# Optimization experiments

Hardware: AMD Instinct MI355X
Metric: run time of the kernel (lower is better)

Reference implementation:

```python
import jax, jax.numpy as jnp
import numpy as np

B, S, E, H = 2, 2048, 1024, 16
D = E // H  # head_dim = 64


def setup_inputs() -> dict:
    key = jax.random.key(0)
    ks = jax.random.split(key, 9)
    sc = 1.0 / np.sqrt(E)
    return {
        "x": jax.random.normal(ks[0], (B, S, E), dtype=jnp.float32),
        "Wq": jax.random.normal(ks[1], (E, E), dtype=jnp.float32) * sc,
        "bq": jnp.zeros((E,), dtype=jnp.float32),
        "Wk": jax.random.normal(ks[2], (E, E), dtype=jnp.float32) * sc,
        "bk": jnp.zeros((E,), dtype=jnp.float32),
        "Wv": jax.random.normal(ks[3], (E, E), dtype=jnp.float32) * sc,
        "bv": jnp.zeros((E,), dtype=jnp.float32),
        "Wo": jax.random.normal(ks[4], (E, E), dtype=jnp.float32) * sc,
        "bo": jnp.zeros((E,), dtype=jnp.float32),
    }


def reference(x, Wq, bq, Wk, bk, Wv, bv, Wo, bo):
    b, s, e = x.shape
    # projections: [B,S,E] -> [B,H,S,D]
    def heads(w, bias):
        return (x @ w + bias).reshape(b, s, H, D).transpose(0, 2, 1, 3)
    q, k, v = heads(Wq, bq), heads(Wk, bk), heads(Wv, bv)
    # scores [B,H,S,S]
    scores = jnp.einsum("bhqd,bhkd->bhqk", q, k) / jnp.sqrt(jnp.float32(D))
    causal = jnp.tril(jnp.ones((s, s), dtype=bool))
    scores = jnp.where(causal[None, None], scores, -jnp.inf)
    weights = jax.nn.softmax(scores, axis=-1)
    out = jnp.einsum("bhqk,bhkd->bhqd", weights, v)
    out = out.transpose(0, 2, 1, 3).reshape(b, s, e)
    return out @ Wo + bo
```

## Files before the change

### kernel.cpp

```cpp
#include <hip/hip_runtime.h>
#include <hip/hip_bf16.h>

#define B_SZ 2
#define S_LEN 2048
#define E_DIM 1024
#define NH 16
#define DH 64
#define M_ROWS (B_SZ * S_LEN)
#define QB 128
#define KVB 64

typedef __attribute__((ext_vector_type(8))) short short8;
typedef __attribute__((ext_vector_type(4))) float floatx4;
typedef __attribute__((ext_vector_type(4))) int intx4;

static __device__ __forceinline__ unsigned short f2bf(float f) {
    __hip_bfloat16 h = __float2bfloat16(f);
    return *reinterpret_cast<unsigned short*>(&h);
}
static __device__ __forceinline__ float bf2f(unsigned short u) {
    unsigned int v = ((unsigned int)u) << 16;
    return __builtin_bit_cast(float, v);
}
static __device__ __forceinline__ unsigned int pack2bf(float lo, float hi) {
    return (unsigned int)f2bf(lo) | ((unsigned int)f2bf(hi) << 16);
}

static __device__ __forceinline__ void gl2lds16(const void* g, void* l) {
    __builtin_amdgcn_global_load_lds((const __attribute__((address_space(1))) void*)g,
                                     (__attribute__((address_space(3))) void*)l, 16, 0, 0);
}

#define WAIT_VM0() asm volatile("s_waitcnt vmcnt(0)" ::: "memory")
#define WAIT_LGKM0() asm volatile("s_waitcnt lgkmcnt(0)" ::: "memory")

__global__ __launch_bounds__(256) void prep(const float* __restrict__ x,
                                            unsigned short* __restrict__ Xb,
                                            const float* __restrict__ W0,
                                            const float* __restrict__ W1,
                                            const float* __restrict__ W2,
                                            const float* __restrict__ W3,
                                            unsigned short* __restrict__ T0,
                                            unsigned short* __restrict__ T1,
                                            unsigned short* __restrict__ T2,
                                            unsigned short* __restrict__ T3) {
    __shared__ float tile[32][33];
    int bid = blockIdx.x;
    int t = threadIdx.x;
    if (bid < 4096) {
        int i = (bid * 256 + t) * 4;
        float4 v = *reinterpret_cast<const float4*>(x + i);
        ushort4 o;
        o.x = f2bf(v.x); o.y = f2bf(v.y); o.z = f2bf(v.z); o.w = f2bf(v.w);
        *reinterpret_cast<ushort4*>(Xb + i) = o;
        return;
    }
    int u = bid - 4096;
    int z = u >> 10, rest = u & 1023;
    int bx = (rest & 31) * 32, by = (rest >> 5) * 32;
    const float* W = (z == 0) ? W0 : (z == 1) ? W1 : (z == 2) ? W2 : W3;
    unsigned short* Wt = (z == 0) ? T0 : (z == 1) ? T1 : (z == 2) ? T2 : T3;
    int tx = t & 31, ty = t >> 5;
#pragma unroll
    for (int i = 0; i < 32; i += 8)
        tile[ty + i][tx] = W[(size_t)(by + ty + i) * E_DIM + bx + tx];
    __syncthreads();
#pragma unroll
    for (int i = 0; i < 32; i += 8)
        Wt[(size_t)(bx + ty + i) * E_DIM + by + tx] = f2bf(tile[tx][ty + i]);
}

#define QSCALE 0.18033688011112042f

__global__ __launch_bounds__(512, 1) void gemm_qkv8(const unsigned short* __restrict__ Wcat,
                                                    const unsigned short* __restrict__ Xb,
                                                    const float* __restrict__ bq,
                                                    const float* __restrict__ bk,
                                                    const float* __restrict__ bv,
                                                    unsigned short* __restrict__ Qg,
                                                    unsigned short* __restrict__ Kg,
                                                    unsigned short* __restrict__ Vtg) {
    __shared__ __align__(16) char lds[2][57344];

    int t = threadIdx.x;
    int b = blockIdx.x;
    int xcd = b & 7, ii = b >> 3;
    int it = (xcd & 3) * 4 + (ii >> 3);
    int jt = (xcd >> 2) * 8 + (ii & 7);
    int iBase = it * 192, jBase = jt << 8;

    int w = t >> 6, lane = t & 63;
    int lr = lane & 15, lh = lane >> 4;
    int wm = w >> 2, wn = w & 3;

    int srow = t >> 3;
    int scbx = ((t & 7) << 4) ^ ((srow & 7) << 4);

    const char* Ab = (const char*)Wcat;
    const char* Bb = (const char*)Xb;

    floatx4 acc[6][4];
#pragma unroll
    for (int i = 0; i < 6; i++)
#pragma unroll
        for (int j = 0; j < 4; j++) acc[i][j] = (floatx4){0.f, 0.f, 0.f, 0.f};

    auto stageA = [&](int buf, int kt) {
        int k0b = kt << 7;
#pragma unroll
        for (int c = 0; c < 3; c++)
            gl2lds16(Ab + (size_t)(iBase + c * 64 + srow) * 2048 + k0b + scbx,
                     &lds[buf][c * 8192 + t * 16]);
    };
    auto stageB = [&](int buf, int kt) {
        int k0b = kt << 7;
#pragma unroll
        for (int c = 0; c < 4; c++)
            gl2lds16(Bb + (size_t)(jBase + c * 64 + srow) * 2048 + k0b + scbx,
                     &lds[buf][24576 + c * 8192 + t * 16]);
    };

    short8 af[3][2], bf[4][2];
    auto rdA = [&](int buf, int qm) {
#pragma unroll
        for (int ml = 0; ml < 3; ml++)
#pragma unroll
            for (int ks = 0; ks < 2; ks++) {
                int row = wm * 96 + (qm * 3 + ml) * 16 + lr;
                af[ml][ks] = *reinterpret_cast<const short8*>(
                    &lds[buf][(row * 128 + ks * 64 + lh * 16) ^ ((row & 7) << 4)]);
            }
    };
    auto rdB = [&](int buf, int qn) {
#pragma unroll
        for (int nl = 0; nl < 2; nl++)
#pragma unroll
            for (int ks = 0; ks < 2; ks++) {
                int row = wn * 64 + (qn * 2 + nl) * 16 + lr;
                bf[qn * 2 + nl][ks] = *reinterpret_cast<const short8*>(
                    &lds[buf][24576 + ((row * 128 + ks * 64 + lh * 16) ^ ((row & 7) << 4))]);
            }
    };
    auto mfma12 = [&](int qm, int qn) {
        __builtin_amdgcn_s_setprio(1);
#pragma unroll
        for (int ml = 0; ml < 3; ml++)
#pragma unroll
            for (int nl = 0; nl < 2; nl++)
#pragma unroll
                for (int ks = 0; ks < 2; ks++)
                    acc[qm * 3 + ml][qn * 2 + nl] = __builtin_amdgcn_mfma_f32_16x16x32_bf16(
                        af[ml][ks], bf[qn * 2 + nl][ks], acc[qm * 3 + ml][qn * 2 + nl], 0, 0, 0);
        __builtin_amdgcn_s_setprio(0);
    };

    const int NT = 16;
    stageA(0, 0);
    stageB(0, 0);
    WAIT_VM0();
    __builtin_amdgcn_s_barrier();

    for (int kt = 0; kt < NT; ++kt) {
        int cur = kt & 1, nxt = cur ^ 1;
        bool pf = (kt + 1 < NT);
        rdA(cur, 0);
        rdB(cur, 0);
        if (pf) stageA(nxt, kt + 1);
        __builtin_amdgcn_s_barrier();
        WAIT_LGKM0();
        __builtin_amdgcn_sched_barrier(0);
        mfma12(0, 0);
        __builtin_amdgcn_s_barrier();
        rdB(cur, 1);
        if (pf) stageB(nxt, kt + 1);
        __builtin_amdgcn_s_barrier();
        WAIT_LGKM0();
        __builtin_amdgcn_sched_barrier(0);
        mfma12(0, 1);
        __builtin_amdgcn_s_barrier();
        rdA(cur, 1);
        __builtin_amdgcn_s_barrier();
        WAIT_LGKM0();
        __builtin_amdgcn_sched_barrier(0);
        mfma12(1, 0);
        __builtin_amdgcn_s_barrier();
        if (pf) WAIT_VM0();
        __builtin_amdgcn_s_barrier();
        mfma12(1, 1);
        __builtin_amdgcn_s_barrier();
    }

    __syncthreads();
    unsigned short* vt = reinterpret_cast<unsigned short*>(&lds[0][0] + w * 2560);

#pragma unroll
    for (int mi = 0; mi < 6; mi++) {
        int i0 = iBase + wm * 96 + mi * 16;
        int wsel = i0 >> 10;
        int im = i0 & 1023;
        const float* bias = (wsel == 0) ? bq : (wsel == 1) ? bk : bv;
        float4 bs = *reinterpret_cast<const float4*>(&bias[im + lh * 4]);
        if (wsel < 2) {
            unsigned short* O = wsel ? Kg : Qg;
            float scale = wsel ? 1.0f : QSCALE;
            int h = im >> 6, d0 = (im & 63) + lh * 4;
#pragma unroll
            for (int nf = 0; nf < 4; nf++) {
                int j = jBase + wn * 64 + nf * 16 + lr;
                int b_ = j >> 11, s = j & (S_LEN - 1);
                ushort4 pk;
                pk.x = f2bf((acc[mi][nf][0] + bs.x) * scale);
                pk.y = f2bf((acc[mi][nf][1] + bs.y) * scale);
                pk.z = f2bf((acc[mi][nf][2] + bs.z) * scale);
                pk.w = f2bf((acc[mi][nf][3] + bs.w) * scale);
                *reinterpret_cast<ushort4*>(
                    &O[((size_t)(b_ * NH + h) * S_LEN + s) * DH + d0]) = pk;
            }
        } else {
#pragma unroll
            for (int nf = 0; nf < 4; nf++)
#pragma unroll
                for (int r = 0; r < 4; r++) {
                    float bb = (r == 0) ? bs.x : (r == 1) ? bs.y : (r == 2) ? bs.z : bs.w;
                    vt[(lh * 4 + r) * 80 + nf * 16 + lr] = f2bf(acc[mi][nf][r] + bb);
                }
            WAIT_LGKM0();
            __builtin_amdgcn_sched_barrier(0);
            int h = im >> 6, d0 = im & 63;
#pragma unroll
            for (int p = 0; p < 2; p++) {
                int idx = p * 64 + lane;
                int dl = idx >> 3, sg = idx & 7;
                short8 vv = *reinterpret_cast<const short8*>(&vt[dl * 80 + sg * 8]);
                int j = jBase + wn * 64 + sg * 8;
                int b_ = j >> 11, s = j & (S_LEN - 1);
                *reinterpret_cast<short8*>(
                    &Vtg[((size_t)(b_ * NH + h) * DH + d0 + dl) * S_LEN + s]) = vv;
            }
            WAIT_LGKM0();
            __builtin_amdgcn_sched_barrier(0);
        }
    }
}

__global__ __launch_bounds__(512, 2) void gemm_o8(const unsigned short* __restrict__ Wot,
                                                  const unsigned short* __restrict__ Og,
                                                  const float* __restrict__ bo,
                                                  float* __restrict__ out) {
    __shared__ __align__(16) char lds[2][2][16384];

    int t = threadIdx.x;
    int b = blockIdx.x;
    int xcd = b & 7, ii = b >> 3;
    int it = ii & 7;
    int jt = (xcd << 2) | (ii >> 3);
    int iBase = it << 7, jBase = jt << 7;

    int w = t >> 6, lane = t & 63;
    int lr = lane & 15, lh = lane >> 4;
    int wm = w >> 2, wn = w & 3;

    int srow = t >> 3;
    int scbx = ((t & 7) << 4) ^ ((srow & 7) << 4);

    const char* Ab = (const char*)Wot;
    const char* Bb = (const char*)Og;

    floatx4 acc[4][2];
#pragma unroll
    for (int i = 0; i < 4; i++)
#pragma unroll
        for (int j = 0; j < 2; j++) acc[i][j] = (floatx4){0.f, 0.f, 0.f, 0.f};

    auto stageA = [&](int buf, int kt) {
        int k0b = kt << 7;
#pragma unroll
        for (int c = 0; c < 2; c++)
            gl2lds16(Ab + (size_t)(iBase + c * 64 + srow) * 2048 + k0b + scbx,
                     &lds[buf][0][c * 8192 + t * 16]);
    };
    auto stageB = [&](int buf, int kt) {
        int k0b = kt << 7;
#pragma unroll
        for (int c = 0; c < 2; c++)
            gl2lds16(Bb + (size_t)(jBase + c * 64 + srow) * 2048 + k0b + scbx,
                     &lds[buf][1][c * 8192 + t * 16]);
    };

    short8 af[4][2], bf[2][2];
    auto rdA = [&](int buf, int qm) {
#pragma unroll
        for (int m2 = 0; m2 < 2; m2++)
#pragma unroll
            for (int ks = 0; ks < 2; ks++) {
                int mi = qm * 2 + m2;
                int row = wm * 64 + mi * 16 + lr;
                af[mi][ks] = *reinterpret_cast<const short8*>(
                    &lds[buf][0][(row * 128 + ks * 64 + lh * 16) ^ ((row & 7) << 4)]);
            }
    };
    auto rdB = [&](int buf) {
#pragma unroll
        for (int nf = 0; nf < 2; nf++)
#pragma unroll
            for (int ks = 0; ks < 2; ks++) {
                int row = wn * 32 + nf * 16 + lr;
                bf[nf][ks] = *reinterpret_cast<const short8*>(
                    &lds[buf][1][(row * 128 + ks * 64 + lh * 16) ^ ((row & 7) << 4)]);
            }
    };
    auto mfma8 = [&](int qm) {
        __builtin_amdgcn_s_setprio(1);
#pragma unroll
        for (int m2 = 0; m2 < 2; m2++)
#pragma unroll
            for (int nf = 0; nf < 2; nf++)
#pragma unroll
                for (int ks = 0; ks < 2; ks++) {
                    int mi = qm * 2 + m2;
                    acc[mi][nf] = __builtin_amdgcn_mfma_f32_16x16x32_bf16(
                        af[mi][ks], bf[nf][ks], acc[mi][nf], 0, 0, 0);
                }
        __builtin_amdgcn_s_setprio(0);
    };

    const int NT = 16;
    stageA(0, 0);
    stageB(0, 0);
    WAIT_VM0();
    __builtin_amdgcn_s_barrier();

    for (int kt = 0; kt < NT; ++kt) {
        int cur = kt & 1, nxt = cur ^ 1;
        bool pf = (kt + 1 < NT);
        rdA(cur, 0);
        rdB(cur);
        if (pf) stageA(nxt, kt + 1);
        __builtin_amdgcn_s_barrier();
        WAIT_LGKM0();
        __builtin_amdgcn_sched_barrier(0);
        mfma8(0);
        __builtin_amdgcn_s_barrier();
        rdA(cur, 1);
        if (pf) stageB(nxt, kt + 1);
        __builtin_amdgcn_s_barrier();
        WAIT_LGKM0();
        __builtin_amdgcn_sched_barrier(0);
        mfma8(1);
        if (pf) WAIT_VM0();
        __builtin_amdgcn_s_barrier();
    }

#pragma unroll
    for (int mi = 0; mi < 4; mi++) {
        int i = iBase + wm * 64 + mi * 16 + lh * 4;
        float4 bs = *reinterpret_cast<const float4*>(&bo[i]);
#pragma unroll
        for (int nf = 0; nf < 2; nf++) {
            int j = jBase + wn * 32 + nf * 16 + lr;
            float4 o;
            o.x = acc[mi][nf][0] + bs.x;
            o.y = acc[mi][nf][1] + bs.y;
            o.z = acc[mi][nf][2] + bs.z;
            o.w = acc[mi][nf][3] + bs.w;
            *reinterpret_cast<float4*>(&out[(size_t)j * E_DIM + i]) = o;
        }
    }
}

__global__ __launch_bounds__(256, 4) void attn_fwd(const unsigned short* __restrict__ Qg,
                                                   const unsigned short* __restrict__ Kg,
                                                   const unsigned short* __restrict__ Vtg,
                                                   unsigned short* __restrict__ Og,
                                                   unsigned short* __restrict__ Opart,
                                                   float* __restrict__ lpart) {
    __shared__ __align__(16) char kt_lds[2][KVB * 128];
    __shared__ __align__(16) char vt_lds[2][KVB * 128];

    int bid = blockIdx.x;
    int xcd = bid & 7, ii = bid >> 3;
    int bh = (xcd << 2) + ii / 30;
    int jj = 29 - (ii % 30);
    int qb, ch, c;
    if (jj < 6)        { qb = jj; ch = 0; c = 1; }
    else if (jj < 18)  { int u = jj - 6;  qb = 6 + (u >> 1); ch = u & 1; c = 2; }
    else               { int u = jj - 18; qb = 12 + u / 3;   ch = u % 3; c = 3; }
    int T = 2 * qb + 2;
    int kt_lo = ch * T / c;
    int kt_hi = (ch + 1) * T / c - 1;
    bool split = (c > 1);

    int w = threadIdx.x >> 6, lane = threadIdx.x & 63;
    int lr = lane & 15, lh = lane >> 4;
    int q0 = qb * QB + w * 32;

    const char* Kb = (const char*)(Kg + (size_t)bh * S_LEN * DH);
    const char* Vb = (const char*)(Vtg + (size_t)bh * DH * S_LEN);
    const unsigned short* Qb = Qg + (size_t)bh * S_LEN * DH;

    int wi0 = w * 2;
    int srow0 = wi0 * 8 + (lane >> 3);
    int scol = (lane & 7) << 4;

    auto stage = [&](int buf, int kt) {
        int kv0 = kt * KVB;
#pragma unroll
        for (int i = 0; i < 2; ++i) {
            int row = srow0 + i * 8;
            int colb = scol ^ ((row & 7) << 4);
            gl2lds16(Kb + (size_t)(kv0 + row) * 128 + colb,
                     kt_lds[buf] + (wi0 + i) * 1024);
            gl2lds16(Vb + (size_t)row * (S_LEN * 2) + (size_t)kv0 * 2 + colb,
                     vt_lds[buf] + (wi0 + i) * 1024);
        }
    };

    short8 aq[2][2];
#pragma unroll
    for (int m = 0; m < 2; m++)
#pragma unroll
        for (int ks = 0; ks < 2; ks++)
            aq[m][ks] = *reinterpret_cast<const short8*>(
                Qb + (size_t)(q0 + m * 16 + lr) * DH + ks * 32 + lh * 8);

    floatx4 oacc[2][4];
    float lsum[2];
#pragma unroll
    for (int m = 0; m < 2; m++) {
#pragma unroll
        for (int dt = 0; dt < 4; dt++) oacc[m][dt] = (floatx4){0.f, 0.f, 0.f, 0.f};
        lsum[m] = 0.f;
    }

    stage(0, kt_lo);
    __syncthreads();
    int buf = 0;

    for (int kt = kt_lo; kt <= kt_hi; ++kt) {
        if (kt < kt_hi) stage(buf ^ 1, kt + 1);
        int kv0 = kt * KVB;
        bool skip = (kv0 > q0 + 31);
        if (!skip) {
            const char* Kt = kt_lds[buf];
            const char* Vt = vt_lds[buf];
            floatx4 sacc[2][4];
#pragma unroll
            for (int m = 0; m < 2; m++)
#pragma unroll
                for (int nt = 0; nt < 4; nt++) sacc[m][nt] = (floatx4){0.f, 0.f, 0.f, 0.f};
#pragma unroll
            for (int ks = 0; ks < 2; ks++)
#pragma unroll
                for (int nt = 0; nt < 4; nt++) {
                    int row = nt * 16 + lr;
                    int addr = (row * 128 + ks * 64 + lh * 16) ^ ((row & 7) << 4);
                    short8 bk = *reinterpret_cast<const short8*>(Kt + addr);
#pragma unroll
                    for (int m = 0; m < 2; m++)
                        sacc[m][nt] = __builtin_amdgcn_mfma_f32_16x16x32_bf16(
                            bk, aq[m][ks], sacc[m][nt], 0, 0, 0);
                }
            if (kv0 + KVB - 1 > q0) {
#pragma unroll
                for (int m = 0; m < 2; m++)
#pragma unroll
                    for (int nt = 0; nt < 4; nt++)
#pragma unroll
                        for (int r = 0; r < 4; r++) {
                            int kcol = kv0 + nt * 16 + lh * 4 + r;
                            int qrow = q0 + m * 16 + lr;
                            if (kcol > qrow) sacc[m][nt][r] = -1e30f;
                        }
            }
            unsigned int pk[2][4][2];
#pragma unroll
            for (int m = 0; m < 2; m++) {
                float ls = 0.f;
#pragma unroll
                for (int nt = 0; nt < 4; nt++) {
#pragma unroll
                    for (int r = 0; r < 4; r++) {
                        float p = __builtin_amdgcn_exp2f(sacc[m][nt][r]);
                        sacc[m][nt][r] = p;
                        ls += p;
                    }
                    pk[m][nt][0] = pack2bf(sacc[m][nt][0], sacc[m][nt][1]);
                    pk[m][nt][1] = pack2bf(sacc[m][nt][2], sacc[m][nt][3]);
                }
                lsum[m] += ls;
            }
            short8 pa[2][2];
            int hsel = lh >> 1;
#pragma unroll
            for (int m = 0; m < 2; m++)
#pragma unroll
                for (int ks = 0; ks < 2; ks++) {
                    intx4 u;
#pragma unroll
                    for (int t4 = 0; t4 < 4; t4++) {
                        int src = lr + 32 * (lh & 1) + 16 * (t4 >> 1);
                        int r0 = __shfl((int)pk[m][2 * ks][t4 & 1], src);
                        int r1 = __shfl((int)pk[m][2 * ks + 1][t4 & 1], src);
                        u[t4] = hsel ? r1 : r0;
                    }
                    pa[m][ks] = __builtin_bit_cast(short8, u);
                }
#pragma unroll
            for (int ks = 0; ks < 2; ks++)
#pragma unroll
                for (int dt = 0; dt < 4; dt++) {
                    int row = dt * 16 + lr;
                    int addr = (row * 128 + ks * 64 + lh * 16) ^ ((row & 7) << 4);
                    short8 bv = *reinterpret_cast<const short8*>(Vt + addr);
#pragma unroll
                    for (int m = 0; m < 2; m++)
                        oacc[m][dt] = __builtin_amdgcn_mfma_f32_16x16x32_bf16(
                            pa[m][ks], bv, oacc[m][dt], 0, 0, 0);
                }
        }
        __syncthreads();
        buf ^= 1;
    }

#pragma unroll
    for (int m = 0; m < 2; m++) {
        lsum[m] += __shfl_xor(lsum[m], 16);
        lsum[m] += __shfl_xor(lsum[m], 32);
    }

    if (split) {
        int base = (qb < 12) ? (qb - 6) * 2 : 12 + (qb - 12) * 3;
        int pi = bh * 24 + base + ch;
        unsigned short* Op = Opart + (size_t)pi * (QB * DH);
        float* lp = lpart + (size_t)pi * QB;
#pragma unroll
        for (int m = 0; m < 2; m++) {
            if (lh == 0) lp[w * 32 + m * 16 + lr] = lsum[m];
#pragma unroll
            for (int r = 0; r < 4; r++) {
                int row = w * 32 + m * 16 + lh * 4 + r;
#pragma unroll
                for (int dt = 0; dt < 4; dt++)
                    Op[row * DH + dt * 16 + lr] = f2bf(oacc[m][dt][r]);
            }
        }
    } else {
        int b_ = bh >> 4, h_ = bh & 15;
#pragma unroll
        for (int m = 0; m < 2; m++) {
#pragma unroll
            for (int r = 0; r < 4; r++) {
                float lv = __shfl(lsum[m], lh * 4 + r);
                float inv = 1.f / lv;
                int srow = q0 + m * 16 + lh * 4 + r;
#pragma unroll
                for (int dt = 0; dt < 4; dt++)
                    Og[((size_t)b_ * S_LEN + srow) * E_DIM + h_ * 64 + dt * 16 + lr] =
                        f2bf(oacc[m][dt][r] * inv);
            }
        }
    }
}

__global__ __launch_bounds__(256) void attn_reduce(const unsigned short* __restrict__ Opart,
                                                   const float* __restrict__ lpart,
                                                   unsigned short* __restrict__ Og) {
    int bh = blockIdx.x;
    int qb = 6 + blockIdx.y;
    int c = (qb < 12) ? 2 : 3;
    int base = (qb < 12) ? (qb - 6) * 2 : 12 + (qb - 12) * 3;
    int pi0 = bh * 24 + base;
    const unsigned short* P0 = Opart + (size_t)pi0 * (QB * DH);
    const float* l0 = lpart + (size_t)pi0 * QB;
    int t = threadIdx.x;
    int cg = t & 7, r0 = t >> 3;
    int b_ = bh >> 4, h_ = bh & 15;
    int qrow0 = qb * QB;
#pragma unroll
    for (int rr = 0; rr < 4; rr++) {
        int row = r0 + rr * 32;
        float ls = l0[row] + l0[QB + row];
        if (c == 3) ls += l0[2 * QB + row];
        float inv = 1.f / ls;
        short8 v0 = *reinterpret_cast<const short8*>(P0 + row * DH + cg * 8);
        short8 v1 = *reinterpret_cast<const short8*>(P0 + QB * DH + row * DH + cg * 8);
        float s[8];
#pragma unroll
        for (int j = 0; j < 8; j++)
            s[j] = bf2f((unsigned short)v0[j]) + bf2f((unsigned short)v1[j]);
        if (c == 3) {
            short8 v2 = *reinterpret_cast<const short8*>(P0 + 2 * QB * DH + row * DH + cg * 8);
#pragma unroll
            for (int j = 0; j < 8; j++) s[j] += bf2f((unsigned short)v2[j]);
        }
        short8 o;
#pragma unroll
        for (int j = 0; j < 8; j++) o[j] = (short)f2bf(s[j] * inv);
        *reinterpret_cast<short8*>(Og + ((size_t)b_ * S_LEN + qrow0 + row) * E_DIM +
                                   h_ * 64 + cg * 8) = o;
    }
}

extern "C" void kernel_launch(void* const* d_in, const int* in_sizes, int n_in,
                              void* d_out, int out_size, void* d_ws, size_t ws_size,
                              hipStream_t stream) {
    const float* x  = (const float*)d_in[0];
    const float* Wq = (const float*)d_in[1];
    const float* bq = (const float*)d_in[2];
    const float* Wk = (const float*)d_in[3];
    const float* bk = (const float*)d_in[4];
    const float* Wv = (const float*)d_in[5];
    const float* bv = (const float*)d_in[6];
    const float* Wo = (const float*)d_in[7];
    const float* bo = (const float*)d_in[8];
    float* out = (float*)d_out;

    const size_t NX = (size_t)M_ROWS * E_DIM;
    const size_t NW = (size_t)E_DIM * E_DIM;
    unsigned short* ws  = (unsigned short*)d_ws;
    unsigned short* Xb  = ws;
    unsigned short* Wqt = Xb + NX;
    unsigned short* Wkt = Wqt + NW;
    unsigned short* Wvt = Wkt + NW;
    unsigned short* Wot = Wvt + NW;
    unsigned short* Qg  = Wot + NW;
    unsigned short* Kg  = Qg + NX;
    unsigned short* Vtg = Kg + NX;
    unsigned short* Og  = Vtg + NX;
    unsigned short* Opart = Xb;
    float* lpart = (float*)(Opart + (size_t)32 * 24 * QB * DH);

    prep<<<dim3(8192), 256, 0, stream>>>(x, Xb, Wq, Wk, Wv, Wo, Wqt, Wkt, Wvt, Wot);

    gemm_qkv8<<<dim3(256), 512, 0, stream>>>(Wqt, Xb, bq, bk, bv, Qg, Kg, Vtg);

    attn_fwd<<<dim3(960), 256, 0, stream>>>(Qg, Kg, Vtg, Og, Opart, lpart);
    attn_reduce<<<dim3(B_SZ * NH, 10), 256, 0, stream>>>(Opart, lpart, Og);

    gemm_o8<<<dim3(256), 512, 0, stream>>>(Wot, Og, bo, out);
}
```

Measured before the change: 107.1 us.

## Balance causal attention work with table-driven multi-segment blocks per head

```diff
diff --git a/kernel.cpp b/kernel.cpp
--- a/kernel.cpp
+++ b/kernel.cpp
@@ -9,6 +9,7 @@
 #define M_ROWS (B_SZ * S_LEN)
 #define QB 128
 #define KVB 64
+#define NSLOT 34
 
 typedef __attribute__((ext_vector_type(8))) short short8;
 typedef __attribute__((ext_vector_type(4))) float floatx4;
@@ -368,31 +369,40 @@
     }
 }
 
+static __device__ const signed char SEG_QB[24][3] = {
+    {0,1,2},{2,3,4},{4,5,-1},{5,6,-1},{6,-1,-1},{7,-1,-1},{7,8,-1},{8,-1,-1},
+    {9,-1,-1},{9,10,-1},{10,-1,-1},{10,11,-1},{11,-1,-1},{11,12,-1},{12,-1,-1},{12,-1,-1},
+    {12,13,-1},{13,-1,-1},{13,14,-1},{14,-1,-1},{14,-1,-1},{14,15,-1},{15,-1,-1},{15,-1,-1}};
+static __device__ const signed char SEG_LO[24][3] = {
+    {0,0,0},{5,0,0},{2,0,0},{4,0,0},{3,0,0},{0,0,0},{12,0,0},{7,0,0},
+    {0,0,0},{12,0,0},{3,0,0},{14,0,0},{4,0,0},{15,0,0},{2,0,0},{14,0,0},
+    {25,0,0},{10,0,0},{22,0,0},{5,0,0},{16,0,0},{28,0,0},{9,0,0},{20,0,0}};
+static __device__ const signed char SEG_HI[24][3] = {
+    {2,4,5},{6,8,2},{10,4,0},{12,3,0},{14,0,0},{12,0,0},{16,7,0},{18,0,0},
+    {12,0,0},{20,3,0},{14,0,0},{22,4,0},{15,0,0},{24,2,0},{14,0,0},{25,0,0},
+    {26,10,0},{22,0,0},{28,5,0},{16,0,0},{28,0,0},{30,9,0},{20,0,0},{32,0,0}};
+static __device__ const signed char SEG_SLOT[24][3] = {
+    {-1,-1,0},{1,-1,2},{3,4,0},{5,6,0},{7,0,0},{8,0,0},{9,10,0},{11,0,0},
+    {12,0,0},{13,14,0},{15,0,0},{16,17,0},{18,0,0},{19,20,0},{21,0,0},{22,0,0},
+    {23,24,0},{25,0,0},{26,27,0},{28,0,0},{29,0,0},{30,31,0},{32,0,0},{33,0,0}};
+
 __global__ __launch_bounds__(256, 4) void attn_fwd(const unsigned short* __restrict__ Qg,
                                                    const unsigned short* __restrict__ Kg,
                                                    const unsigned short* __restrict__ Vtg,
                                                    unsigned short* __restrict__ Og,
-                                                   unsigned short* __restrict__ Opart,
+                                                   unsigned short* __restrict__ OpA,
+                                                   unsigned short* __restrict__ OpB,
                                                    float* __restrict__ lpart) {
     __shared__ __align__(16) char kt_lds[2][KVB * 128];
     __shared__ __align__(16) char vt_lds[2][KVB * 128];
 
     int bid = blockIdx.x;
     int xcd = bid & 7, ii = bid >> 3;
-    int bh = (xcd << 2) + ii / 30;
-    int jj = 29 - (ii % 30);
-    int qb, ch, c;
-    if (jj < 6)        { qb = jj; ch = 0; c = 1; }
-    else if (jj < 18)  { int u = jj - 6;  qb = 6 + (u >> 1); ch = u & 1; c = 2; }
-    else               { int u = jj - 18; qb = 12 + u / 3;   ch = u % 3; c = 3; }
-    int T = 2 * qb + 2;
-    int kt_lo = ch * T / c;
-    int kt_hi = (ch + 1) * T / c - 1;
-    bool split = (c > 1);
+    int bh = (xcd << 2) + ii / 24;
+    int c = ii % 24;
 
     int w = threadIdx.x >> 6, lane = threadIdx.x & 63;
     int lr = lane & 15, lh = lane >> 4;
-    int q0 = qb * QB + w * 32;
 
     const char* Kb = (const char*)(Kg + (size_t)bh * S_LEN * DH);
     const char* Vb = (const char*)(Vtg + (size_t)bh * DH * S_LEN);
@@ -415,163 +425,173 @@
         }
     };
 
-    short8 aq[2][2];
-#pragma unroll
-    for (int m = 0; m < 2; m++)
-#pragma unroll
-        for (int ks = 0; ks < 2; ks++)
-            aq[m][ks] = *reinterpret_cast<const short8*>(
-                Qb + (size_t)(q0 + m * 16 + lr) * DH + ks * 32 + lh * 8);
-
-    floatx4 oacc[2][4];
-    float lsum[2];
-#pragma unroll
-    for (int m = 0; m < 2; m++) {
-#pragma unroll
-        for (int dt = 0; dt < 4; dt++) oacc[m][dt] = (floatx4){0.f, 0.f, 0.f, 0.f};
-        lsum[m] = 0.f;
+    for (int si = 0; si < 3; ++si) {
+        int qb = SEG_QB[c][si];
+        if (qb < 0) break;
+        int klo = SEG_LO[c][si], khi = SEG_HI[c][si];
+        int slot = SEG_SLOT[c][si];
+        int q0 = qb * QB + w * 32;
+
+        short8 aq[2][2];
+#pragma unroll
+        for (int m = 0; m < 2; m++)
+#pragma unroll
+            for (int ks = 0; ks < 2; ks++)
+                aq[m][ks] = *reinterpret_cast<const short8*>(
+                    Qb + (size_t)(q0 + m * 16 + lr) * DH + ks * 32 + lh * 8);
+
+        floatx4 oacc[2][4];
+        float lsum[2];
+#pragma unroll
+        for (int m = 0; m < 2; m++) {
+#pragma unroll
+            for (int dt = 0; dt < 4; dt++) oacc[m][dt] = (floatx4){0.f, 0.f, 0.f, 0.f};
+            lsum[m] = 0.f;
+        }
+
+        stage(0, klo);
+        __syncthreads();
+        int buf = 0;
+
+        for (int kt = klo; kt < khi; ++kt) {
+            if (kt + 1 < khi) stage(buf ^ 1, kt + 1);
+            int kv0 = kt * KVB;
+            bool skip = (kv0 > q0 + 31);
+            if (!skip) {
+                const char* Kt = kt_lds[buf];
+                const char* Vt = vt_lds[buf];
+                floatx4 sacc[2][4];
+#pragma unroll
+                for (int m = 0; m < 2; m++)
+#pragma unroll
+                    for (int nt = 0; nt < 4; nt++) sacc[m][nt] = (floatx4){0.f, 0.f, 0.f, 0.f};
+#pragma unroll
+                for (int ks = 0; ks < 2; ks++)
+#pragma unroll
+                    for (int nt = 0; nt < 4; nt++) {
+                        int row = nt * 16 + lr;
+                        int addr = (row * 128 + ks * 64 + lh * 16) ^ ((row & 7) << 4);
+                        short8 bk = *reinterpret_cast<const short8*>(Kt + addr);
+#pragma unroll
+                        for (int m = 0; m < 2; m++)
+                            sacc[m][nt] = __builtin_amdgcn_mfma_f32_16x16x32_bf16(
+                                bk, aq[m][ks], sacc[m][nt], 0, 0, 0);
+                    }
+                if (kv0 + KVB - 1 > q0) {
+#pragma unroll
+                    for (int m = 0; m < 2; m++)
+#pragma unroll
+                        for (int nt = 0; nt < 4; nt++)
+#pragma unroll
+                            for (int r = 0; r < 4; r++) {
+                                int kcol = kv0 + nt * 16 + lh * 4 + r;
+                                int qrow = q0 + m * 16 + lr;
+                                if (kcol > qrow) sacc[m][nt][r] = -1e30f;
+                            }
+                }
+                unsigned int pk[2][4][2];
+#pragma unroll
+                for (int m = 0; m < 2; m++) {
+                    float ls = 0.f;
+#pragma unroll
+                    for (int nt = 0; nt < 4; nt++) {
+#pragma unroll
+                        for (int r = 0; r < 4; r++) {
+                            float p = __builtin_amdgcn_exp2f(sacc[m][nt][r]);
+                            sacc[m][nt][r] = p;
+                            ls += p;
+                        }
+                        pk[m][nt][0] = pack2bf(sacc[m][nt][0], sacc[m][nt][1]);
+                        pk[m][nt][1] = pack2bf(sacc[m][nt][2], sacc[m][nt][3]);
+                    }
+                    lsum[m] += ls;
+                }
+                short8 pa[2][2];
+                int hsel = lh >> 1;
+#pragma unroll
+                for (int m = 0; m < 2; m++)
+#pragma unroll
+                    for (int ks = 0; ks < 2; ks++) {
+                        intx4 u;
+#pragma unroll
+                        for (int t4 = 0; t4 < 4; t4++) {
+                            int src = lr + 32 * (lh & 1) + 16 * (t4 >> 1);
+                            int r0 = __shfl((int)pk[m][2 * ks][t4 & 1], src);
+                            int r1 = __shfl((int)pk[m][2 * ks + 1][t4 & 1], src);
+                            u[t4] = hsel ? r1 : r0;
+                        }
+                        pa[m][ks] = __builtin_bit_cast(short8, u);
+                    }
+#pragma unroll
+                for (int ks = 0; ks < 2; ks++)
+#pragma unroll
+                    for (int dt = 0; dt < 4; dt++) {
+                        int row = dt * 16 + lr;
+                        int addr = (row * 128 + ks * 64 + lh * 16) ^ ((row & 7) << 4);
+                        short8 bv = *reinterpret_cast<const short8*>(Vt + addr);
+#pragma unroll
+                        for (int m = 0; m < 2; m++)
+                            oacc[m][dt] = __builtin_amdgcn_mfma_f32_16x16x32_bf16(
+                                pa[m][ks], bv, oacc[m][dt], 0, 0, 0);
+                    }
+            }
+            __syncthreads();
+            buf ^= 1;
+        }
+
+#pragma unroll
+        for (int m = 0; m < 2; m++) {
+            lsum[m] += __shfl_xor(lsum[m], 16);
+            lsum[m] += __shfl_xor(lsum[m], 32);
+        }
+
+        if (slot >= 0) {
+            int pi = bh * NSLOT + slot;
+            unsigned short* Op = (pi < 896) ? OpA + (size_t)pi * (QB * DH)
+                                            : OpB + (size_t)(pi - 896) * (QB * DH);
+            float* lp = lpart + (size_t)pi * QB;
+#pragma unroll
+            for (int m = 0; m < 2; m++) {
+                if (lh == 0) lp[w * 32 + m * 16 + lr] = lsum[m];
+#pragma unroll
+                for (int r = 0; r < 4; r++) {
+                    int row = w * 32 + m * 16 + lh * 4 + r;
+#pragma unroll
+                    for (int dt = 0; dt < 4; dt++)
+                        Op[row * DH + dt * 16 + lr] = f2bf(oacc[m][dt][r]);
+                }
+            }
+        } else {
+            int b_ = bh >> 4, h_ = bh & 15;
+#pragma unroll
+            for (int m = 0; m < 2; m++) {
+#pragma unroll
+                for (int r = 0; r < 4; r++) {
+                    float lv = __shfl(lsum[m], lh * 4 + r);
+                    float inv = 1.f / lv;
+                    int srw = q0 + m * 16 + lh * 4 + r;
+#pragma unroll
+                    for (int dt = 0; dt < 4; dt++)
+                        Og[((size_t)b_ * S_LEN + srw) * E_DIM + h_ * 64 + dt * 16 + lr] =
+                            f2bf(oacc[m][dt][r] * inv);
+                }
+            }
+        }
     }
-
-    stage(0, kt_lo);
-    __syncthreads();
-    int buf = 0;
-
-    for (int kt = kt_lo; kt <= kt_hi; ++kt) {
-        if (kt < kt_hi) stage(buf ^ 1, kt + 1);
-        int kv0 = kt * KVB;
-        bool skip = (kv0 > q0 + 31);
-        if (!skip) {
-            const char* Kt = kt_lds[buf];
-            const char* Vt = vt_lds[buf];
-            floatx4 sacc[2][4];
-#pragma unroll
-            for (int m = 0; m < 2; m++)
-#pragma unroll
-                for (int nt = 0; nt < 4; nt++) sacc[m][nt] = (floatx4){0.f, 0.f, 0.f, 0.f};
-#pragma unroll
-            for (int ks = 0; ks < 2; ks++)
-#pragma unroll
-                for (int nt = 0; nt < 4; nt++) {
-                    int row = nt * 16 + lr;
-                    int addr = (row * 128 + ks * 64 + lh * 16) ^ ((row & 7) << 4);
-                    short8 bk = *reinterpret_cast<const short8*>(Kt + addr);
-#pragma unroll
-                    for (int m = 0; m < 2; m++)
-                        sacc[m][nt] = __builtin_amdgcn_mfma_f32_16x16x32_bf16(
-                            bk, aq[m][ks], sacc[m][nt], 0, 0, 0);
-                }
-            if (kv0 + KVB - 1 > q0) {
-#pragma unroll
-                for (int m = 0; m < 2; m++)
-#pragma unroll
-                    for (int nt = 0; nt < 4; nt++)
-#pragma unroll
-                        for (int r = 0; r < 4; r++) {
-                            int kcol = kv0 + nt * 16 + lh * 4 + r;
-                            int qrow = q0 + m * 16 + lr;
-                            if (kcol > qrow) sacc[m][nt][r] = -1e30f;
-                        }
-            }
-            unsigned int pk[2][4][2];
-#pragma unroll
-            for (int m = 0; m < 2; m++) {
-                float ls = 0.f;
-#pragma unroll
-                for (int nt = 0; nt < 4; nt++) {
-#pragma unroll
-                    for (int r = 0; r < 4; r++) {
-                        float p = __builtin_amdgcn_exp2f(sacc[m][nt][r]);
-                        sacc[m][nt][r] = p;
-                        ls += p;
-                    }
-                    pk[m][nt][0] = pack2bf(sacc[m][nt][0], sacc[m][nt][1]);
-                    pk[m][nt][1] = pack2bf(sacc[m][nt][2], sacc[m][nt][3]);
-                }
-                lsum[m] += ls;
-            }
-            short8 pa[2][2];
-            int hsel = lh >> 1;
-#pragma unroll
-            for (int m = 0; m < 2; m++)
-#pragma unroll
-                for (int ks = 0; ks < 2; ks++) {
-                    intx4 u;
-#pragma unroll
-                    for (int t4 = 0; t4 < 4; t4++) {
-                        int src = lr + 32 * (lh & 1) + 16 * (t4 >> 1);
-                        int r0 = __shfl((int)pk[m][2 * ks][t4 & 1], src);
-                        int r1 = __shfl((int)pk[m][2 * ks + 1][t4 & 1], src);
-                        u[t4] = hsel ? r1 : r0;
-                    }
-                    pa[m][ks] = __builtin_bit_cast(short8, u);
-                }
-#pragma unroll
-            for (int ks = 0; ks < 2; ks++)
-#pragma unroll
-                for (int dt = 0; dt < 4; dt++) {
-                    int row = dt * 16 + lr;
-                    int addr = (row * 128 + ks * 64 + lh * 16) ^ ((row & 7) << 4);
-                    short8 bv = *reinterpret_cast<const short8*>(Vt + addr);
-#pragma unroll
-                    for (int m = 0; m < 2; m++)
-                        oacc[m][dt] = __builtin_amdgcn_mfma_f32_16x16x32_bf16(
-                            pa[m][ks], bv, oacc[m][dt], 0, 0, 0);
-                }
-        }
-        __syncthreads();
-        buf ^= 1;
-    }
-
-#pragma unroll
-    for (int m = 0; m < 2; m++) {
-        lsum[m] += __shfl_xor(lsum[m], 16);
-        lsum[m] += __shfl_xor(lsum[m], 32);
-    }
-
-    if (split) {
-        int base = (qb < 12) ? (qb - 6) * 2 : 12 + (qb - 12) * 3;
-        int pi = bh * 24 + base + ch;
-        unsigned short* Op = Opart + (size_t)pi * (QB * DH);
-        float* lp = lpart + (size_t)pi * QB;
-#pragma unroll
-        for (int m = 0; m < 2; m++) {
-            if (lh == 0) lp[w * 32 + m * 16 + lr] = lsum[m];
-#pragma unroll
-            for (int r = 0; r < 4; r++) {
-                int row = w * 32 + m * 16 + lh * 4 + r;
-#pragma unroll
-                for (int dt = 0; dt < 4; dt++)
-                    Op[row * DH + dt * 16 + lr] = f2bf(oacc[m][dt][r]);
-            }
-        }
-    } else {
-        int b_ = bh >> 4, h_ = bh & 15;
-#pragma unroll
-        for (int m = 0; m < 2; m++) {
-#pragma unroll
-            for (int r = 0; r < 4; r++) {
-                float lv = __shfl(lsum[m], lh * 4 + r);
-                float inv = 1.f / lv;
-                int srow = q0 + m * 16 + lh * 4 + r;
-#pragma unroll
-                for (int dt = 0; dt < 4; dt++)
-                    Og[((size_t)b_ * S_LEN + srow) * E_DIM + h_ * 64 + dt * 16 + lr] =
-                        f2bf(oacc[m][dt][r] * inv);
-            }
-        }
-    }
-}
-
-__global__ __launch_bounds__(256) void attn_reduce(const unsigned short* __restrict__ Opart,
+}
+
+static __device__ const signed char RQB[13] = {2, 4, 5, 6, 7, 8, 9, 10, 11, 12, 13, 14, 15};
+static __device__ const signed char RS0[13] = {0, 2, 4, 6, 8, 10, 12, 14, 17, 20, 24, 27, 31};
+static __device__ const signed char RC[13]  = {2, 2, 2, 2, 2, 2, 2, 3, 3, 4, 3, 4, 3};
+
+__global__ __launch_bounds__(256) void attn_reduce(const unsigned short* __restrict__ OpA,
+                                                   const unsigned short* __restrict__ OpB,
                                                    const float* __restrict__ lpart,
                                                    unsigned short* __restrict__ Og) {
     int bh = blockIdx.x;
-    int qb = 6 + blockIdx.y;
-    int c = (qb < 12) ? 2 : 3;
-    int base = (qb < 12) ? (qb - 6) * 2 : 12 + (qb - 12) * 3;
-    int pi0 = bh * 24 + base;
-    const unsigned short* P0 = Opart + (size_t)pi0 * (QB * DH);
-    const float* l0 = lpart + (size_t)pi0 * QB;
+    int qy = blockIdx.y;
+    int qb = RQB[qy], s0 = RS0[qy], cnt = RC[qy];
+    int pi0 = bh * NSLOT + s0;
     int t = threadIdx.x;
     int cg = t & 7, r0 = t >> 3;
     int b_ = bh >> 4, h_ = bh & 15;
@@ -579,20 +599,18 @@
 #pragma unroll
     for (int rr = 0; rr < 4; rr++) {
         int row = r0 + rr * 32;
-        float ls = l0[row] + l0[QB + row];
-        if (c == 3) ls += l0[2 * QB + row];
+        float ls = 0.f;
+        float s[8] = {0.f, 0.f, 0.f, 0.f, 0.f, 0.f, 0.f, 0.f};
+        for (int k = 0; k < cnt; k++) {
+            int pi = pi0 + k;
+            const unsigned short* P = (pi < 896) ? OpA + (size_t)pi * (QB * DH)
+                                                 : OpB + (size_t)(pi - 896) * (QB * DH);
+            ls += lpart[(size_t)pi * QB + row];
+            short8 v = *reinterpret_cast<const short8*>(P + row * DH + cg * 8);
+#pragma unroll
+            for (int j = 0; j < 8; j++) s[j] += bf2f((unsigned short)v[j]);
+        }
         float inv = 1.f / ls;
-        short8 v0 = *reinterpret_cast<const short8*>(P0 + row * DH + cg * 8);
-        short8 v1 = *reinterpret_cast<const short8*>(P0 + QB * DH + row * DH + cg * 8);
-        float s[8];
-#pragma unroll
-        for (int j = 0; j < 8; j++)
-            s[j] = bf2f((unsigned short)v0[j]) + bf2f((unsigned short)v1[j]);
-        if (c == 3) {
-            short8 v2 = *reinterpret_cast<const short8*>(P0 + 2 * QB * DH + row * DH + cg * 8);
-#pragma unroll
-            for (int j = 0; j < 8; j++) s[j] += bf2f((unsigned short)v2[j]);
-        }
         short8 o;
 #pragma unroll
         for (int j = 0; j < 8; j++) o[j] = (short)f2bf(s[j] * inv);
@@ -627,15 +645,16 @@
     unsigned short* Kg  = Qg + NX;
     unsigned short* Vtg = Kg + NX;
     unsigned short* Og  = Vtg + NX;
-    unsigned short* Opart = Xb;
-    float* lpart = (float*)(Opart + (size_t)32 * 24 * QB * DH);
+    unsigned short* OpA = Xb;
+    unsigned short* OpB = Og + NX;
+    float* lpart = (float*)(OpB + (size_t)192 * QB * DH);
 
     prep<<<dim3(8192), 256, 0, stream>>>(x, Xb, Wq, Wk, Wv, Wo, Wqt, Wkt, Wvt, Wot);
 
     gemm_qkv8<<<dim3(256), 512, 0, stream>>>(Wqt, Xb, bq, bk, bv, Qg, Kg, Vtg);
 
-    attn_fwd<<<dim3(960), 256, 0, stream>>>(Qg, Kg, Vtg, Og, Opart, lpart);
-    attn_reduce<<<dim3(B_SZ * NH, 10), 256, 0, stream>>>(Opart, lpart, Og);
+    attn_fwd<<<dim3(768), 256, 0, stream>>>(Qg, Kg, Vtg, Og, OpA, OpB, lpart);
+    attn_reduce<<<dim3(32, 13), 256, 0, stream>>>(OpA, OpB, lpart, Og);
 
     gemm_o8<<<dim3(256), 512, 0, stream>>>(Wot, Og, bo, out);
 }
```

Result: slower. 115.4 us (+7.8%).
